# Performance work log

Hardware: AMD Instinct MI355X
Metric: run time of the kernel (lower is better)

## Reference

```python
import jax, jax.numpy as jnp
import numpy as np

HEAD_NUM = 16
HEAD_SIZE = 64
D_MODEL = 1024
B, N = 8, 1024
MASK_PENALTY = 1e8


def setup_inputs() -> dict:
    key = jax.random.key(0)
    k1, k2, k3 = jax.random.split(key, 3)
    inputs = jax.random.normal(k1, (B, N, D_MODEL), dtype=jnp.float32)
    mask = jax.random.randint(k2, (B, N), 0, 2).astype(jnp.float32)
    # glorot-uniform-ish init for kernel [H, 3, d_model, head_size]
    limit = float(np.sqrt(6.0 / (D_MODEL + HEAD_SIZE)))
    kernel = jax.random.uniform(k3, (HEAD_NUM, 3, D_MODEL, HEAD_SIZE),
                                dtype=jnp.float32, minval=-limit, maxval=limit)
    return {"inputs": inputs, "mask": mask, "kernel": kernel}


def reference(inputs, mask, kernel):
    # inputs: [B,N,d], kernel: [H,3,d,s]
    q = jnp.einsum('bnd,hds->bhns', inputs, kernel[:, 0])
    k = jnp.einsum('bnd,hds->bhns', inputs, kernel[:, 1])
    v = jnp.einsum('bnd,hds->bhns', inputs, kernel[:, 2])
    # NOTE: original never applies 1/sqrt(head_size) scaling (faithful).
    scores = jnp.einsum('bhns,bhms->bhnm', q, k)  # [B,H,N,N]
    # additive mask: outer product of padding mask, penalty on masked pairs
    pair_mask = mask[:, None, :, None] * mask[:, None, None, :]  # [B,1,N,N]
    scores = scores - MASK_PENALTY * (1.0 - pair_mask)
    attn = jax.nn.softmax(scores, axis=-1)
    out = jnp.einsum('bhnm,bhms->bhns', attn, v)  # [B,H,N,s]
    # original permutes to [B,N,s,H] then flattens -> head axis fastest
    out = jnp.transpose(out, (0, 2, 3, 1))  # [B,N,s,H]
    return out.reshape(out.shape[0], out.shape[1], HEAD_SIZE * HEAD_NUM)
```

## Files before the change

### kernel.cpp

```cpp
#include <hip/hip_runtime.h>
#include <math.h>

#define BB 8
#define NN 1024
#define DD 1024
#define HH 16
#define SS 64
#define BH (BB*HH)

typedef _Float16 half8 __attribute__((ext_vector_type(8)));
typedef _Float16 half4v __attribute__((ext_vector_type(4)));
typedef float floatx4 __attribute__((ext_vector_type(4)));

#define MFMA16(A, B, C) __builtin_amdgcn_mfma_f32_16x16x32_f16((A), (B), (C), 0, 0, 0)

__device__ __forceinline__ void gload16(const _Float16* g, _Float16* l) {
    __builtin_amdgcn_global_load_lds(
        (const __attribute__((address_space(1))) void*)g,
        (__attribute__((address_space(3))) void*)l,
        16, 0, 0);
}

__global__ __launch_bounds__(256) void split_x(
    const float* __restrict__ X, _Float16* __restrict__ Xh, _Float16* __restrict__ Xl)
{
    int idx = (blockIdx.x * 256 + threadIdx.x) * 4;
    float4 x4 = *(const float4*)(X + idx);
    float xs[4] = {x4.x, x4.y, x4.z, x4.w};
    half4v h, l;
    #pragma unroll
    for (int i = 0; i < 4; i++) {
        _Float16 hi = (_Float16)xs[i];
        h[i] = hi;
        l[i] = (_Float16)(xs[i] - (float)hi);
    }
    *(half4v*)(Xh + idx) = h;
    *(half4v*)(Xl + idx) = l;
}

__global__ __launch_bounds__(256) void split_wt(
    const float* __restrict__ W, _Float16* __restrict__ Wth, _Float16* __restrict__ Wtl)
{
    __shared__ float tile[64][68];
    const int hc = blockIdx.x, d0 = blockIdx.y * 64;
    const int t = threadIdx.x;
    {
        int i = t >> 2, sq = (t & 3) * 16;
        const float* src = W + ((size_t)hc * DD + d0 + i) * SS + sq;
        #pragma unroll
        for (int u = 0; u < 4; u++) {
            float4 v = *(const float4*)(src + 4 * u);
            tile[i][sq + 4 * u + 0] = v.x; tile[i][sq + 4 * u + 1] = v.y;
            tile[i][sq + 4 * u + 2] = v.z; tile[i][sq + 4 * u + 3] = v.w;
        }
    }
    __syncthreads();
    {
        int s = t >> 2, jq = (t & 3) * 16;
        _Float16 hbuf[16], lbuf[16];
        #pragma unroll
        for (int u = 0; u < 16; u++) {
            float x = tile[jq + u][s];
            _Float16 hi = (_Float16)x;
            hbuf[u] = hi;
            lbuf[u] = (_Float16)(x - (float)hi);
        }
        size_t off = (size_t)hc * SS * DD + (size_t)s * DD + d0 + jq;
        *(half8*)(Wth + off)     = *(half8*)(hbuf);
        *(half8*)(Wth + off + 8) = *(half8*)(hbuf + 8);
        *(half8*)(Wtl + off)     = *(half8*)(lbuf);
        *(half8*)(Wtl + off + 8) = *(half8*)(lbuf + 8);
    }
}

__global__ __launch_bounds__(256, 2) void qkv_mfma(
    const _Float16* __restrict__ Xh, const _Float16* __restrict__ Xl,
    const _Float16* __restrict__ Wth, const _Float16* __restrict__ Wtl,
    _Float16* __restrict__ Qh, _Float16* __restrict__ Ql,
    _Float16* __restrict__ Kh, _Float16* __restrict__ Kl,
    _Float16* __restrict__ Vt)
{
    const int flat = blockIdx.y * 64 + blockIdx.x;
    const int swz  = (flat & 7) * 192 + (flat >> 3);
    const int bx = swz & 63;
    const int by = swz >> 6;
    const int cvar = by % 3;
    const int hp   = by / 3;
    const int hc_w0 = (2 * hp) * 3 + cvar;
    const int r0  = bx * 128;

    const int tid = threadIdx.x;
    const int wave = tid >> 6, lane = tid & 63;
    const int l16 = lane & 15, quad = lane >> 4;
    const int wr = wave >> 1, wc = wave & 1;

    __shared__ _Float16 sAh[128 * 32];
    __shared__ _Float16 sAl[128 * 32];
    __shared__ _Float16 sBh[128 * 32];
    __shared__ _Float16 sBl[128 * 32];

    floatx4 acc[4][4];
    #pragma unroll
    for (int i = 0; i < 4; i++)
        #pragma unroll
        for (int j = 0; j < 4; j++) acc[i][j] = (floatx4){0.f, 0.f, 0.f, 0.f};

    const _Float16* Ab_h = Xh  + (size_t)r0 * DD;
    const _Float16* Ab_l = Xl  + (size_t)r0 * DD;
    const _Float16* Bb_h = Wth + (size_t)hc_w0 * SS * DD;
    const _Float16* Bb_l = Wtl + (size_t)hc_w0 * SS * DD;

    for (int k0 = 0; k0 < DD; k0 += 32) {
        #pragma unroll
        for (int i = 0; i < 2; i++) {
            const int g = tid + 256 * i;
            const int row = g >> 2, kc = (g & 3) * 8;
            const size_t go = (size_t)row * DD + k0 + kc;
            const size_t bo = go + ((row & 64) ? (size_t)(2 * SS * DD) : 0);
            gload16(Ab_h + go, &sAh[g * 8]);
            if (cvar != 2) gload16(Ab_l + go, &sAl[g * 8]);
            gload16(Bb_h + bo, &sBh[g * 8]);
            gload16(Bb_l + bo, &sBl[g * 8]);
        }
        __syncthreads();

        half8 Ah[4], Al[4], Bh[4], Bl[4];
        #pragma unroll
        for (int t = 0; t < 4; t++) {
            const int ar = wr * 64 + 16 * t + l16;
            const int br = wc * 64 + 16 * t + l16;
            Ah[t] = *(const half8*)&sAh[ar * 32 + quad * 8];
            Bh[t] = *(const half8*)&sBh[br * 32 + quad * 8];
            Bl[t] = *(const half8*)&sBl[br * 32 + quad * 8];
        }
        if (cvar != 2) {
            #pragma unroll
            for (int t = 0; t < 4; t++) {
                const int ar = wr * 64 + 16 * t + l16;
                Al[t] = *(const half8*)&sAl[ar * 32 + quad * 8];
            }
        }
        #pragma unroll
        for (int i = 0; i < 4; i++)
            #pragma unroll
            for (int j = 0; j < 4; j++)
                acc[i][j] = MFMA16(Ah[i], Bh[j], acc[i][j]);
        #pragma unroll
        for (int i = 0; i < 4; i++)
            #pragma unroll
            for (int j = 0; j < 4; j++)
                acc[i][j] = MFMA16(Ah[i], Bl[j], acc[i][j]);
        if (cvar != 2) {
            #pragma unroll
            for (int i = 0; i < 4; i++)
                #pragma unroll
                for (int j = 0; j < 4; j++)
                    acc[i][j] = MFMA16(Al[i], Bh[j], acc[i][j]);
        }
        __syncthreads();
    }

    const int h = 2 * hp + wc;
    const int c = cvar;
    const int rowbase = r0 + wr * 64;
    if (c == 2) {
        #pragma unroll
        for (int i = 0; i < 4; i++)
            #pragma unroll
            for (int j = 0; j < 4; j++) {
                int tok0 = rowbase + 16 * i + 4 * quad;
                int b = tok0 >> 10, n0 = tok0 & 1023;
                half4v pk;
                #pragma unroll
                for (int r = 0; r < 4; r++) pk[r] = (_Float16)acc[i][j][r];
                *(half4v*)(Vt + ((size_t)(b * HH + h) * SS + 16 * j + l16) * NN + n0) = pk;
            }
    } else {
        _Float16* Ph = (c == 0) ? Qh : Kh;
        _Float16* Pl = (c == 0) ? Ql : Kl;
        #pragma unroll
        for (int i = 0; i < 4; i++)
            #pragma unroll
            for (int j = 0; j < 4; j++)
                #pragma unroll
                for (int r = 0; r < 4; r++) {
                    int tok = rowbase + 16 * i + 4 * quad + r;
                    int b = tok >> 10, n = tok & 1023;
                    float v = acc[i][j][r];
                    _Float16 vh = (_Float16)v;
                    _Float16 vl = (_Float16)(v - (float)vh);
                    size_t off = ((size_t)(b * HH + h) * NN + n) * SS + 16 * j + l16;
                    Ph[off] = vh; Pl[off] = vl;
                }
    }
}

__global__ __launch_bounds__(512) void attn_mfma(
    const _Float16* __restrict__ Qh, const _Float16* __restrict__ Ql,
    const _Float16* __restrict__ Kh, const _Float16* __restrict__ Kl,
    const _Float16* __restrict__ Vt,
    const float* __restrict__ mask,
    float* __restrict__ out)
{
    const int bh = blockIdx.x, qt = blockIdx.y;
    const int b = bh >> 4, h = bh & 15;
    const int tid = threadIdx.x;
    const int wave = tid >> 6, lane = tid & 63;
    const int l16 = lane & 15, quad = lane >> 4;

    __shared__ float Ms[NN];
    __shared__ _Float16 KhS[64 * 64];
    __shared__ _Float16 KlS[64 * 64];
    __shared__ _Float16 VS [64 * 64];
    __shared__ _Float16 Plds[8][32][72];

    *(float2*)&Ms[tid * 2] = *(const float2*)(mask + b * NN + tid * 2);

    half8 G[3];
    auto stage_load = [&](int kt_) {
        int g = tid;
        int row = g >> 3;
        int c = (g & 7) ^ (row & 7);
        size_t ko = ((size_t)bh * NN + kt_ * 64 + row) * SS + c * 8;
        G[0] = *(const half8*)(Kh + ko);
        G[1] = *(const half8*)(Kl + ko);
        G[2] = *(const half8*)(Vt + ((size_t)bh * SS + row) * NN
                               + (size_t)kt_ * 64 + c * 8);
    };
    auto stage_store = [&]() {
        int g = tid;
        *(half8*)&KhS[g * 8] = G[0];
        *(half8*)&KlS[g * 8] = G[1];
        *(half8*)&VS [g * 8] = G[2];
    };

    stage_load(0);
    stage_store();
    __syncthreads();

    const int qrow0 = qt * 256 + wave * 32;
    half8 Aqh[2][2], Aql[2][2];
    #pragma unroll
    for (int g = 0; g < 2; g++) {
        const size_t qbase = ((size_t)bh * NN + qrow0 + 16 * g + l16) * SS + quad * 8;
        Aqh[g][0] = *(const half8*)(Qh + qbase);
        Aqh[g][1] = *(const half8*)(Qh + qbase + 32);
        Aql[g][0] = *(const half8*)(Ql + qbase);
        Aql[g][1] = *(const half8*)(Ql + qbase + 32);
    }

    float qm[2], m_old[2], l_sum[2];
    floatx4 accO[2][4];
    #pragma unroll
    for (int g = 0; g < 2; g++) {
        qm[g] = Ms[qrow0 + 16 * g + l16];
        m_old[g] = -3.0e38f;
        l_sum[g] = 0.f;
        #pragma unroll
        for (int j = 0; j < 4; j++) accO[g][j] = (floatx4){0.f, 0.f, 0.f, 0.f};
    }

    const int sw = l16 & 7;

    for (int kt = 0; kt < 16; kt++) {
        if (kt < 15) stage_load(kt + 1);

        floatx4 accS[2][4];
        #pragma unroll
        for (int g = 0; g < 2; g++)
            #pragma unroll
            for (int jt = 0; jt < 4; jt++) accS[g][jt] = (floatx4){0.f, 0.f, 0.f, 0.f};
        __builtin_amdgcn_s_setprio(1);
        #pragma unroll
        for (int jt = 0; jt < 4; jt++) {
            const int rowK = jt * 16 + l16;
            const _Float16* krh = &KhS[rowK * 64];
            const _Float16* krl = &KlS[rowK * 64];
            half8 Bh0 = *(const half8*)&krh[((quad    ) ^ sw) * 8];
            half8 Bh1 = *(const half8*)&krh[((quad + 4) ^ sw) * 8];
            half8 Bl0 = *(const half8*)&krl[((quad    ) ^ sw) * 8];
            half8 Bl1 = *(const half8*)&krl[((quad + 4) ^ sw) * 8];
            #pragma unroll
            for (int g = 0; g < 2; g++) {
                accS[g][jt] = MFMA16(Bh0, Aqh[g][0], accS[g][jt]);
                accS[g][jt] = MFMA16(Bh1, Aqh[g][1], accS[g][jt]);
                accS[g][jt] = MFMA16(Bl0, Aqh[g][0], accS[g][jt]);
                accS[g][jt] = MFMA16(Bl1, Aqh[g][1], accS[g][jt]);
                accS[g][jt] = MFMA16(Bh0, Aql[g][0], accS[g][jt]);
                accS[g][jt] = MFMA16(Bh1, Aql[g][1], accS[g][jt]);
            }
        }
        __builtin_amdgcn_s_setprio(0);

        float km[4][4];
        #pragma unroll
        for (int jt = 0; jt < 4; jt++) {
            float4 k4 = *(const float4*)&Ms[kt * 64 + jt * 16 + quad * 4];
            km[jt][0] = k4.x; km[jt][1] = k4.y; km[jt][2] = k4.z; km[jt][3] = k4.w;
        }
        #pragma unroll
        for (int g = 0; g < 2; g++)
            #pragma unroll
            for (int jt = 0; jt < 4; jt++)
                #pragma unroll
                for (int r = 0; r < 4; r++)
                    accS[g][jt][r] -= 1.0e8f * (1.0f - qm[g] * km[jt][r]);

        #pragma unroll
        for (int g = 0; g < 2; g++) {
            float a0 = fmaxf(fmaxf(accS[g][0][0], accS[g][0][1]),
                             fmaxf(accS[g][0][2], accS[g][0][3]));
            float a1 = fmaxf(fmaxf(accS[g][1][0], accS[g][1][1]),
                             fmaxf(accS[g][1][2], accS[g][1][3]));
            float a2 = fmaxf(fmaxf(accS[g][2][0], accS[g][2][1]),
                             fmaxf(accS[g][2][2], accS[g][2][3]));
            float a3 = fmaxf(fmaxf(accS[g][3][0], accS[g][3][1]),
                             fmaxf(accS[g][3][2], accS[g][3][3]));
            float mt = fmaxf(fmaxf(a0, a1), fmaxf(a2, a3));
            mt = fmaxf(mt, __shfl_xor(mt, 16, 64));
            mt = fmaxf(mt, __shfl_xor(mt, 32, 64));
            float mn = fmaxf(m_old[g], mt);

            float sj[4];
            #pragma unroll
            for (int jt = 0; jt < 4; jt++) {
                float p0 = __expf(accS[g][jt][0] - mn);
                float p1 = __expf(accS[g][jt][1] - mn);
                float p2 = __expf(accS[g][jt][2] - mn);
                float p3 = __expf(accS[g][jt][3] - mn);
                accS[g][jt][0] = p0; accS[g][jt][1] = p1;
                accS[g][jt][2] = p2; accS[g][jt][3] = p3;
                sj[jt] = (p0 + p1) + (p2 + p3);
            }
            float ls = (sj[0] + sj[1]) + (sj[2] + sj[3]);
            ls += __shfl_xor(ls, 16, 64);
            ls += __shfl_xor(ls, 32, 64);

            if (__any(mt > m_old[g])) {
                float alpha = __expf(m_old[g] - mn);
                m_old[g] = mn;
                l_sum[g] = l_sum[g] * alpha + ls;
                float alphaO[4];
                #pragma unroll
                for (int r = 0; r < 4; r++)
                    alphaO[r] = __shfl(alpha, quad * 4 + r, 64);
                #pragma unroll
                for (int j = 0; j < 4; j++)
                    #pragma unroll
                    for (int r = 0; r < 4; r++)
                        accO[g][j][r] *= alphaO[r];
            } else {
                l_sum[g] = l_sum[g] + ls;
            }

            #pragma unroll
            for (int jt = 0; jt < 4; jt++) {
                half4v pk;
                #pragma unroll
                for (int r = 0; r < 4; r++) pk[r] = (_Float16)accS[g][jt][r];
                *(half4v*)&Plds[wave][16 * g + l16][jt * 16 + quad * 4] = pk;
            }
        }

        __builtin_amdgcn_s_setprio(1);
        #pragma unroll
        for (int ks = 0; ks < 2; ks++) {
            half8 Ap[2];
            #pragma unroll
            for (int g = 0; g < 2; g++)
                Ap[g] = *(const half8*)&Plds[wave][16 * g + l16][ks * 32 + quad * 8];
            #pragma unroll
            for (int j = 0; j < 4; j++) {
                half8 Bv = *(const half8*)&VS[(j * 16 + l16) * 64
                                              + (((ks * 4 + quad) ^ sw) * 8)];
                #pragma unroll
                for (int g = 0; g < 2; g++)
                    accO[g][j] = MFMA16(Ap[g], Bv, accO[g][j]);
            }
        }
        __builtin_amdgcn_s_setprio(0);

        if (kt < 15) {
            __syncthreads();
            stage_store();
            __syncthreads();
        }
    }

    #pragma unroll
    for (int g = 0; g < 2; g++) {
        float inv[4];
        #pragma unroll
        for (int r = 0; r < 4; r++)
            inv[r] = 1.f / __shfl(l_sum[g], quad * 4 + r, 64);
        #pragma unroll
        for (int r = 0; r < 4; r++) {
            int qrow = qrow0 + 16 * g + quad * 4 + r;
            #pragma unroll
            for (int j = 0; j < 4; j++)
                out[((size_t)(b * NN + qrow)) * (SS * HH) + (j * 16 + l16) * HH + h] =
                    accO[g][j][r] * inv[r];
        }
    }
}

__global__ __launch_bounds__(256) void qkv_kernel(
    const float* __restrict__ X, const float* __restrict__ W, float* __restrict__ qkv)
{
    const int ttile = blockIdx.x;
    const int hc    = blockIdx.y;
    const int h     = hc / 3, c = hc % 3;
    const int tid = threadIdx.x;
    const int tx = tid & 15, ty = tid >> 4;
    __shared__ float As[32][68];
    __shared__ float Bs[32][68];
    const float* Wb = W + (size_t)hc * DD * SS;
    const int row0 = ttile * 64;
    float acc[4][4];
    #pragma unroll
    for (int i = 0; i < 4; i++)
        #pragma unroll
        for (int j = 0; j < 4; j++) acc[i][j] = 0.f;
    for (int k0 = 0; k0 < DD; k0 += 32) {
        #pragma unroll
        for (int l = 0; l < 2; l++) {
            int i = tid + l * 256;
            int r = i >> 3;
            int kq = (i & 7) * 4;
            float4 x4 = *(const float4*)(X + (size_t)(row0 + r) * DD + k0 + kq);
            As[kq + 0][r] = x4.x; As[kq + 1][r] = x4.y;
            As[kq + 2][r] = x4.z; As[kq + 3][r] = x4.w;
        }
        #pragma unroll
        for (int l = 0; l < 2; l++) {
            int i = tid + l * 256;
            int kr = i >> 4;
            int sq = (i & 15) * 4;
            *(float4*)&Bs[kr][sq] = *(const float4*)(Wb + (size_t)(k0 + kr) * SS + sq);
        }
        __syncthreads();
        #pragma unroll
        for (int kk = 0; kk < 32; kk++) {
            float4 a4 = *(const float4*)&As[kk][ty * 4];
            float4 b4 = *(const float4*)&Bs[kk][tx * 4];
            float a[4] = {a4.x, a4.y, a4.z, a4.w};
            float bb[4] = {b4.x, b4.y, b4.z, b4.w};
            #pragma unroll
            for (int i = 0; i < 4; i++)
                #pragma unroll
                for (int j = 0; j < 4; j++)
                    acc[i][j] = fmaf(a[i], bb[j], acc[i][j]);
        }
        __syncthreads();
    }
    float* outp = qkv + (size_t)c * BH * NN * SS;
    #pragma unroll
    for (int i = 0; i < 4; i++) {
        int tg = row0 + ty * 4 + i;
        int b = tg >> 10, n = tg & 1023;
        float4 v4 = make_float4(acc[i][0], acc[i][1], acc[i][2], acc[i][3]);
        *(float4*)(outp + ((size_t)(b * HH + h) * NN + n) * SS + tx * 4) = v4;
    }
}

__global__ __launch_bounds__(256) void attn_kernel(
    const float* __restrict__ qkv,
    const float* __restrict__ mask,
    float* __restrict__ out)
{
    const int qt = blockIdx.x, h = blockIdx.y, b = blockIdx.z;
    const int tid = threadIdx.x;
    const int tx = tid & 15, ty = tid >> 4;
    const int bh = b * HH + h;
    const float* Q = qkv + (size_t)bh * NN * SS;
    const float* K = qkv + (size_t)BH * NN * SS + (size_t)bh * NN * SS;
    const float* V = qkv + 2 * (size_t)BH * NN * SS + (size_t)bh * NN * SS;

    __shared__ float QsT[64][68];
    __shared__ float KsT[64][68];
    __shared__ float Vs [64][68];
    __shared__ float PsT[64][68];
    __shared__ float Ms[NN];

    {
        float4 mm = *(const float4*)(mask + b * NN + tid * 4);
        *(float4*)&Ms[tid * 4] = mm;
    }
    #pragma unroll
    for (int l = 0; l < 4; l++) {
        int i = tid + l * 256;
        int r = i >> 4, sq = (i & 15) * 4;
        float4 x4 = *(const float4*)(Q + (size_t)(qt * 64 + r) * SS + sq);
        QsT[sq + 0][r] = x4.x; QsT[sq + 1][r] = x4.y;
        QsT[sq + 2][r] = x4.z; QsT[sq + 3][r] = x4.w;
    }
    __syncthreads();

    float m_old[4], l_sum[4], O[4][4], qm[4];
    #pragma unroll
    for (int i = 0; i < 4; i++) {
        qm[i] = Ms[qt * 64 + ty * 4 + i];
        m_old[i] = -3.0e38f; l_sum[i] = 0.f;
        #pragma unroll
        for (int j = 0; j < 4; j++) O[i][j] = 0.f;
    }

    for (int kt = 0; kt < 16; kt++) {
        #pragma unroll
        for (int l = 0; l < 4; l++) {
            int i = tid + l * 256;
            int r = i >> 4, sq = (i & 15) * 4;
            float4 k4 = *(const float4*)(K + (size_t)(kt * 64 + r) * SS + sq);
            KsT[sq + 0][r] = k4.x; KsT[sq + 1][r] = k4.y;
            KsT[sq + 2][r] = k4.z; KsT[sq + 3][r] = k4.w;
            float4 v4 = *(const float4*)(V + (size_t)(kt * 64 + r) * SS + sq);
            *(float4*)&Vs[r][sq] = v4;
        }
        __syncthreads();

        float sc[4][4];
        #pragma unroll
        for (int i = 0; i < 4; i++)
            #pragma unroll
            for (int j = 0; j < 4; j++) sc[i][j] = 0.f;
        #pragma unroll 8
        for (int s = 0; s < 64; s++) {
            float4 a4 = *(const float4*)&QsT[s][ty * 4];
            float4 b4 = *(const float4*)&KsT[s][tx * 4];
            float a[4] = {a4.x, a4.y, a4.z, a4.w};
            float bb[4] = {b4.x, b4.y, b4.z, b4.w};
            #pragma unroll
            for (int i = 0; i < 4; i++)
                #pragma unroll
                for (int j = 0; j < 4; j++)
                    sc[i][j] = fmaf(a[i], bb[j], sc[i][j]);
        }
        float km[4];
        #pragma unroll
        for (int j = 0; j < 4; j++) km[j] = Ms[kt * 64 + tx * 4 + j];
        #pragma unroll
        for (int i = 0; i < 4; i++)
            #pragma unroll
            for (int j = 0; j < 4; j++) {
                float pen = 1.0e8f * (1.0f - qm[i] * km[j]);
                sc[i][j] = sc[i][j] - pen;
            }

        #pragma unroll
        for (int i = 0; i < 4; i++) {
            float mt = fmaxf(fmaxf(sc[i][0], sc[i][1]), fmaxf(sc[i][2], sc[i][3]));
            #pragma unroll
            for (int off = 1; off < 16; off <<= 1)
                mt = fmaxf(mt, __shfl_xor(mt, off, 64));
            float mn = fmaxf(m_old[i], mt);
            float alpha = __expf(m_old[i] - mn);
            float p[4];
            #pragma unroll
            for (int j = 0; j < 4; j++) p[j] = __expf(sc[i][j] - mn);
            float ls = (p[0] + p[1]) + (p[2] + p[3]);
            #pragma unroll
            for (int off = 1; off < 16; off <<= 1)
                ls += __shfl_xor(ls, off, 64);
            l_sum[i] = l_sum[i] * alpha + ls;
            m_old[i] = mn;
            #pragma unroll
            for (int j = 0; j < 4; j++) {
                O[i][j] *= alpha;
                PsT[tx * 4 + j][ty * 4 + i] = p[j];
            }
        }
        __syncthreads();

        #pragma unroll 8
        for (int kj = 0; kj < 64; kj++) {
            float4 p4 = *(const float4*)&PsT[kj][ty * 4];
            float4 v4 = *(const float4*)&Vs[kj][tx * 4];
            float p[4] = {p4.x, p4.y, p4.z, p4.w};
            float vv[4] = {v4.x, v4.y, v4.z, v4.w};
            #pragma unroll
            for (int i = 0; i < 4; i++)
                #pragma unroll
                for (int j = 0; j < 4; j++)
                    O[i][j] = fmaf(p[i], vv[j], O[i][j]);
        }
        __syncthreads();
    }

    #pragma unroll
    for (int i = 0; i < 4; i++) {
        int qrow = qt * 64 + ty * 4 + i;
        float inv = 1.f / l_sum[i];
        #pragma unroll
        for (int j = 0; j < 4; j++) {
            int s = tx * 4 + j;
            out[((size_t)(b * NN + qrow)) * (SS * HH) + s * HH + h] = O[i][j] * inv;
        }
    }
}

extern "C" void kernel_launch(void* const* d_in, const int* in_sizes, int n_in,
                              void* d_out, int out_size, void* d_ws, size_t ws_size,
                              hipStream_t stream) {
    const float* X    = (const float*)d_in[0];
    const float* mask = (const float*)d_in[1];
    const float* W    = (const float*)d_in[2];
    float* out = (float*)d_out;

    const size_t x_elems  = (size_t)BB * NN * DD;
    const size_t w_elems  = (size_t)HH * 3 * SS * DD;
    const size_t qk_elems = (size_t)BH * NN * SS;
    const size_t need_fast = (2 * x_elems + 2 * w_elems + 5 * qk_elems) * sizeof(_Float16);

    if (ws_size >= need_fast) {
        _Float16* Xh  = (_Float16*)d_ws;
        _Float16* Xl  = Xh  + x_elems;
        _Float16* Wth = Xl  + x_elems;
        _Float16* Wtl = Wth + w_elems;
        _Float16* Qh  = Wtl + w_elems;
        _Float16* Ql  = Qh  + qk_elems;
        _Float16* Kh  = Ql  + qk_elems;
        _Float16* Kl  = Kh  + qk_elems;
        _Float16* Vt  = Kl  + qk_elems;

        split_x<<<dim3((unsigned)(x_elems / 1024)), dim3(256), 0, stream>>>(X, Xh, Xl);
        split_wt<<<dim3(48, 16), dim3(256), 0, stream>>>(W, Wth, Wtl);
        qkv_mfma<<<dim3(64, 24), dim3(256), 0, stream>>>(Xh, Xl, Wth, Wtl, Qh, Ql, Kh, Kl, Vt);
        attn_mfma<<<dim3(128, 4), dim3(512), 0, stream>>>(Qh, Ql, Kh, Kl, Vt, mask, out);
    } else if (ws_size >= 3ull * BH * NN * SS * sizeof(float)) {
        float* qkv = (float*)d_ws;
        qkv_kernel<<<dim3(128, 48), dim3(256), 0, stream>>>(X, W, qkv);
        attn_kernel<<<dim3(16, 16, 8), dim3(256), 0, stream>>>(qkv, mask, out);
    }
}
```

Before: 407.7 us.

## Double-buffer K/V tiles in LDS and drop one barrier per tile

Doubles the LDS buffers for the Kh/Kl/V tiles so the next tile can be stored while other waves still read the current one, which removes the barrier before the store in each key-tile iteration. Also moves the P·V MFMA step inside the per-row-group loop, so the per-wave P staging buffer only holds 16 rows instead of 32. Total LDS per block grows somewhat. Handling the two row groups one after the other may reduce MFMA interleaving between them.

```diff
diff --git a/kernel.cpp b/kernel.cpp
--- a/kernel.cpp
+++ b/kernel.cpp
@@ -209,10 +209,10 @@
     const int l16 = lane & 15, quad = lane >> 4;
 
     __shared__ float Ms[NN];
-    __shared__ _Float16 KhS[64 * 64];
-    __shared__ _Float16 KlS[64 * 64];
-    __shared__ _Float16 VS [64 * 64];
-    __shared__ _Float16 Plds[8][32][72];
+    __shared__ _Float16 KhS[2][64 * 64];
+    __shared__ _Float16 KlS[2][64 * 64];
+    __shared__ _Float16 VS [2][64 * 64];
+    __shared__ _Float16 Plds[8][16][72];
 
     *(float2*)&Ms[tid * 2] = *(const float2*)(mask + b * NN + tid * 2);
 
@@ -227,15 +227,15 @@
         G[2] = *(const half8*)(Vt + ((size_t)bh * SS + row) * NN
                                + (size_t)kt_ * 64 + c * 8);
     };
-    auto stage_store = [&]() {
+    auto stage_store = [&](int buf) {
         int g = tid;
-        *(half8*)&KhS[g * 8] = G[0];
-        *(half8*)&KlS[g * 8] = G[1];
-        *(half8*)&VS [g * 8] = G[2];
+        *(half8*)&KhS[buf][g * 8] = G[0];
+        *(half8*)&KlS[buf][g * 8] = G[1];
+        *(half8*)&VS [buf][g * 8] = G[2];
     };
 
     stage_load(0);
-    stage_store();
+    stage_store(0);
     __syncthreads();
 
     const int qrow0 = qt * 256 + wave * 32;
@@ -263,6 +263,7 @@
     const int sw = l16 & 7;
 
     for (int kt = 0; kt < 16; kt++) {
+        const int cur = kt & 1;
         if (kt < 15) stage_load(kt + 1);
 
         floatx4 accS[2][4];
@@ -274,8 +275,8 @@
         #pragma unroll
         for (int jt = 0; jt < 4; jt++) {
             const int rowK = jt * 16 + l16;
-            const _Float16* krh = &KhS[rowK * 64];
-            const _Float16* krl = &KlS[rowK * 64];
+            const _Float16* krh = &KhS[cur][rowK * 64];
+            const _Float16* krl = &KlS[cur][rowK * 64];
             half8 Bh0 = *(const half8*)&krh[((quad    ) ^ sw) * 8];
             half8 Bh1 = *(const half8*)&krh[((quad + 4) ^ sw) * 8];
             half8 Bl0 = *(const half8*)&krl[((quad    ) ^ sw) * 8];
@@ -358,31 +359,25 @@
                 half4v pk;
                 #pragma unroll
                 for (int r = 0; r < 4; r++) pk[r] = (_Float16)accS[g][jt][r];
-                *(half4v*)&Plds[wave][16 * g + l16][jt * 16 + quad * 4] = pk;
-            }
-        }
-
-        __builtin_amdgcn_s_setprio(1);
-        #pragma unroll
-        for (int ks = 0; ks < 2; ks++) {
-            half8 Ap[2];
-            #pragma unroll
-            for (int g = 0; g < 2; g++)
-                Ap[g] = *(const half8*)&Plds[wave][16 * g + l16][ks * 32 + quad * 8];
-            #pragma unroll
-            for (int j = 0; j < 4; j++) {
-                half8 Bv = *(const half8*)&VS[(j * 16 + l16) * 64
-                                              + (((ks * 4 + quad) ^ sw) * 8)];
-                #pragma unroll
-                for (int g = 0; g < 2; g++)
-                    accO[g][j] = MFMA16(Ap[g], Bv, accO[g][j]);
-            }
-        }
-        __builtin_amdgcn_s_setprio(0);
+                *(half4v*)&Plds[wave][l16][jt * 16 + quad * 4] = pk;
+            }
+
+            __builtin_amdgcn_s_setprio(1);
+            #pragma unroll
+            for (int ks = 0; ks < 2; ks++) {
+                half8 Ap = *(const half8*)&Plds[wave][l16][ks * 32 + quad * 8];
+                #pragma unroll
+                for (int j = 0; j < 4; j++) {
+                    half8 Bv = *(const half8*)&VS[cur][(j * 16 + l16) * 64
+                                                       + (((ks * 4 + quad) ^ sw) * 8)];
+                    accO[g][j] = MFMA16(Ap, Bv, accO[g][j]);
+                }
+            }
+            __builtin_amdgcn_s_setprio(0);
+        }
 
         if (kt < 15) {
-            __syncthreads();
-            stage_store();
+            stage_store(cur ^ 1);
             __syncthreads();
         }
     }
```

New measurement: 406.7 us. About the same (-0.2%).
